# Kernel tuning notes

Measured on AMD Instinct MI355X. Metric: run time of the kernel, lower is better.

## Reference

```python
import jax, jax.numpy as jnp
import numpy as np

N = 500_000   # active voxel sites
C = 128       # inplanes == outplanes
K = 4         # 2x2 submanifold filter offsets
EPS = 1e-4    # SCN BatchNorm default eps


def setup_inputs() -> dict:
    key = jax.random.key(0)
    ks = jax.random.split(key, 10)
    feat = jax.random.normal(ks[0], (N, C), jnp.float32)
    in_idx = jax.random.randint(ks[1], (K, N), 0, N, dtype=jnp.int32)
    out_idx = jax.random.randint(ks[2], (K, N), 0, N, dtype=jnp.int32)
    mask = jax.random.randint(ks[3], (K, N), 0, 2, dtype=jnp.int32)
    scale = 1.0 / np.sqrt(K * C)
    W1 = jax.random.normal(ks[4], (K, C, C), jnp.float32) * scale
    W2 = jax.random.normal(ks[5], (K, C, C), jnp.float32) * scale
    gamma1 = jnp.ones((C,), jnp.float32)
    beta1 = jnp.zeros((C,), jnp.float32)
    mean1 = jax.random.normal(ks[6], (C,), jnp.float32) * 0.1
    var1 = jax.random.uniform(ks[7], (C,), jnp.float32, 0.5, 1.5)
    gamma2 = jnp.ones((C,), jnp.float32)
    beta2 = jnp.zeros((C,), jnp.float32)
    mean2 = jax.random.normal(ks[8], (C,), jnp.float32) * 0.1
    var2 = jax.random.uniform(ks[9], (C,), jnp.float32, 0.5, 1.5)
    return dict(feat=feat, W1=W1, W2=W2, gamma1=gamma1, beta1=beta1,
                mean1=mean1, var1=var1, gamma2=gamma2, beta2=beta2,
                mean2=mean2, var2=var2, in_idx=in_idx, out_idx=out_idx, mask=mask)


def _subm_conv(feat, W, in_idx, out_idx, maskf):
    # rulebook gather -> GEMM -> scatter-add, one pass per kernel offset
    out = jnp.zeros((feat.shape[0], W.shape[-1]), feat.dtype)
    for k in range(W.shape[0]):  # K=4 fixed small offsets
        g = feat[in_idx[k]] * maskf[k][:, None]   # [N, Cin]
        out = out.at[out_idx[k]].add(g @ W[k])    # scatter to active sites
    return out


def _bn(x, gamma, beta, mean, var):
    return (x - mean) * jax.lax.rsqrt(var + EPS) * gamma + beta


def reference(feat, W1, W2, gamma1, beta1, mean1, var1,
              gamma2, beta2, mean2, var2, in_idx, out_idx, mask):
    maskf = mask.astype(feat.dtype)
    residual = feat                              # scn.Identity (stride=1)
    h = _subm_conv(feat, W1, in_idx, out_idx, maskf)
    h = jax.nn.relu(_bn(h, gamma1, beta1, mean1, var1))  # BatchNormReLU
    h = _subm_conv(h, W2, in_idx, out_idx, maskf)
    h = _bn(h, gamma2, beta2, mean2, var2)       # BatchNormalization
    return h + residual                          # AddTable
```

## Files before the change

### kernel.cpp

```cpp
#include <hip/hip_runtime.h>

#define CDIM 128
#define KOFF 4
#define EPS 1e-4f
#define SCAN_CHUNK 2048
#define ROWS 32
#define NBLK 512
#define NTHR 512
#define CAPM (1 << 18)

typedef __attribute__((ext_vector_type(8))) short bf16x8;
typedef __attribute__((ext_vector_type(4))) float f32x4;

__device__ __forceinline__ unsigned short f2bf(float f) {
    unsigned int u = __builtin_bit_cast(unsigned int, f);
    u += 0x7fffu + ((u >> 16) & 1u);
    return (unsigned short)(u >> 16);
}
__device__ __forceinline__ float bf2f(unsigned short h) {
    unsigned int u = ((unsigned int)h) << 16;
    return __builtin_bit_cast(float, u);
}

__device__ __forceinline__ void gload_lds16(const void* g, void* l) {
    __builtin_amdgcn_global_load_lds(
        (const __attribute__((address_space(1))) void*)g,
        (__attribute__((address_space(3))) void*)l, 16, 0, 0);
}

__global__ __launch_bounds__(256) void wconv_kernel(
    const float* __restrict__ W1, const float* __restrict__ W2,
    short* __restrict__ W1t, short* __restrict__ W2t)
{
    int idx = blockIdx.x * 256 + threadIdx.x;
    if (idx >= KOFF * CDIM * CDIM) return;
    int ci = idx & (CDIM - 1);
    int co = (idx >> 7) & (CDIM - 1);
    int k  = idx >> 14;
    size_t src = (size_t)k * CDIM * CDIM + (size_t)ci * CDIM + co;
    W1t[idx] = (short)f2bf(W1[src]);
    W2t[idx] = (short)f2bf(W2[src]);
}

__global__ __launch_bounds__(256) void cvt_kernel(
    const float* __restrict__ in, short* __restrict__ out, size_t total8)
{
    size_t stride = (size_t)gridDim.x * 256;
    for (size_t i = (size_t)blockIdx.x * 256 + threadIdx.x; i < total8; i += stride) {
        float4 a = ((const float4*)in)[i * 2];
        float4 b = ((const float4*)in)[i * 2 + 1];
        bf16x8 v;
        v[0] = (short)f2bf(a.x); v[1] = (short)f2bf(a.y);
        v[2] = (short)f2bf(a.z); v[3] = (short)f2bf(a.w);
        v[4] = (short)f2bf(b.x); v[5] = (short)f2bf(b.y);
        v[6] = (short)f2bf(b.z); v[7] = (short)f2bf(b.w);
        ((bf16x8*)out)[i] = v;
    }
}

__global__ __launch_bounds__(256) void count_kernel(
    const int* __restrict__ out_idx, const int* __restrict__ mask,
    int* __restrict__ cnt, int n)
{
    int i = blockIdx.x * 256 + threadIdx.x;
    if (i >= n) return;
    int k = blockIdx.y;
    size_t s = (size_t)k * n + i;
    if (mask[s]) atomicAdd(&cnt[(size_t)out_idx[s] * KOFF + k], 1);
}

__global__ __launch_bounds__(256) void scan_p1(
    const int* __restrict__ in, int* __restrict__ bsum, int* __restrict__ bsum2, int L)
{
    __shared__ int red[256], red2[256];
    int base = blockIdx.x * SCAN_CHUNK;
    int s = 0, m = 0;
    #pragma unroll
    for (int u = 0; u < 8; ++u) {
        int i = base + u * 256 + threadIdx.x;
        if (i < L) { int v = in[i]; s += v; m += (v >= 2); }
    }
    red[threadIdx.x] = s; red2[threadIdx.x] = m;
    __syncthreads();
    for (int d = 128; d > 0; d >>= 1) {
        if (threadIdx.x < d) {
            red[threadIdx.x]  += red[threadIdx.x + d];
            red2[threadIdx.x] += red2[threadIdx.x + d];
        }
        __syncthreads();
    }
    if (threadIdx.x == 0) { bsum[blockIdx.x] = red[0]; bsum2[blockIdx.x] = red2[0]; }
}

__global__ __launch_bounds__(1024) void scan_p2(
    int* __restrict__ bsum, int* __restrict__ bsum2, int NB)
{
    __shared__ int s[1024], s2[1024];
    int t = threadIdx.x;
    s[t]  = (t < NB) ? bsum[t]  : 0;
    s2[t] = (t < NB) ? bsum2[t] : 0;
    __syncthreads();
    for (int d = 1; d < 1024; d <<= 1) {
        int x = s[t], y = s2[t];
        if (t >= d) { x += s[t - d]; y += s2[t - d]; }
        __syncthreads();
        s[t] = x; s2[t] = y;
        __syncthreads();
    }
    if (t < NB) {
        bsum[t]  = (t == 0) ? 0 : s[t - 1];
        bsum2[t] = (t == 0) ? 0 : s2[t - 1];
    }
}

__global__ __launch_bounds__(256) void scan_p3(
    const int* __restrict__ cnt, const int* __restrict__ bsum,
    const int* __restrict__ bsum2, int* __restrict__ off_start,
    int* __restrict__ fcur, int* __restrict__ prim,
    int* __restrict__ mlist, int* __restrict__ nmulti, int L, int KN)
{
    __shared__ int ts[256], ms[256];
    int t = threadIdx.x;
    int base = blockIdx.x * SCAN_CHUNK + t * 8;
    int v[8]; int s = 0, m = 0;
    #pragma unroll
    for (int u = 0; u < 8; ++u) {
        int i = base + u;
        v[u] = (i < L) ? cnt[i] : 0;
        s += v[u]; m += (v[u] >= 2);
    }
    ts[t] = s; ms[t] = m;
    __syncthreads();
    for (int d = 1; d < 256; d <<= 1) {
        int x = ts[t], y = ms[t];
        if (t >= d) { x += ts[t - d]; y += ms[t - d]; }
        __syncthreads();
        ts[t] = x; ms[t] = y;
        __syncthreads();
    }
    int pre  = bsum[blockIdx.x]  + ((t == 0) ? 0 : ts[t - 1]);
    int mpre = bsum2[blockIdx.x] + ((t == 0) ? 0 : ms[t - 1]);
    #pragma unroll
    for (int u = 0; u < 8; ++u) {
        int i = base + u;
        if (i < L) {
            off_start[i] = pre;
            fcur[i] = pre;
            if (i < KN) {
                int c = v[u];
                if (c == 0) prim[i] = -1;
                else if (c >= 2) {
                    if (mpre < CAPM) { prim[i] = 0x40000000 | mpre; mlist[mpre] = i; }
                    else prim[i] = -1;
                }
            } else {
                nmulti[0] = mpre;
            }
            pre += v[u]; mpre += (v[u] >= 2);
        }
    }
}

__global__ __launch_bounds__(256) void fill_kernel(
    const int* __restrict__ out_idx, const int* __restrict__ in_idx,
    const int* __restrict__ mask, const int* __restrict__ cnt,
    int* __restrict__ fcur, int* __restrict__ ent, int* __restrict__ prim, int n)
{
    int i = blockIdx.x * 256 + threadIdx.x;
    if (i >= n) return;
    int k = blockIdx.y;
    size_t s = (size_t)k * n + i;
    if (mask[s]) {
        int j = out_idx[s];
        size_t b = (size_t)j * KOFF + k;
        int src = in_idx[s];
        if (cnt[b] == 1) prim[b] = src;
        else { int pos = atomicAdd(&fcur[b], 1); ent[pos] = src; }
    }
}

__global__ __launch_bounds__(256) void merge_kernel(
    const short* __restrict__ Xb, const int* __restrict__ off_start,
    const int* __restrict__ ent, const int* __restrict__ mlist,
    const int* __restrict__ nmulti, short* __restrict__ sumbuf)
{
    int nm = *nmulti; if (nm > CAPM) nm = CAPM;
    int grp  = (blockIdx.x * 256 + threadIdx.x) >> 5;
    int gl   = threadIdx.x & 31;
    int ngrp = (gridDim.x * 256) >> 5;
    for (int i = grp; i < nm; i += ngrp) {
        int b  = mlist[i];
        int e0 = off_start[b];
        int e1 = off_start[b + 1];
        float a0 = 0.f, a1 = 0.f, a2 = 0.f, a3 = 0.f;
        for (int e = e0; e < e1; ++e) {
            int src = ent[e];
            ushort4 v = *((const ushort4*)(Xb + (size_t)src * CDIM) + gl);
            a0 += bf2f(v.x); a1 += bf2f(v.y); a2 += bf2f(v.z); a3 += bf2f(v.w);
        }
        ushort4 o;
        o.x = f2bf(a0); o.y = f2bf(a1); o.z = f2bf(a2); o.w = f2bf(a3);
        *((ushort4*)(sumbuf + (size_t)i * CDIM) + gl) = o;
    }
}

template <int EPI>
__global__ __launch_bounds__(NTHR, 4) void conv_kernel(
    const short* __restrict__ Xb, const short* __restrict__ sumbuf,
    const short* __restrict__ Wt, const int* __restrict__ prim,
    const char* __restrict__ zpage,
    const float* __restrict__ gamma, const float* __restrict__ beta,
    const float* __restrict__ mean, const float* __restrict__ var,
    const float* __restrict__ feat, void* __restrict__ Yv,
    int n, int ntile, int tpb)
{
    const int t    = threadIdx.x;
    const int w    = t >> 6;
    const int lane = t & 63;

    __shared__ alignas(16) short As[2][ROWS * 512];
    __shared__ alignas(16) float s_scale[CDIM], s_shift[CDIM];

    if (t < CDIM) {
        float sc = gamma[t] * rsqrtf(var[t] + EPS);
        s_scale[t] = sc;
        s_shift[t] = beta[t] - mean[t] * sc;
    }
    __syncthreads();

    int t0 = blockIdx.x * tpb;
    int t1 = min(t0 + tpb, ntile);
    if (t0 >= t1) return;

    const int q    = lane >> 4;
    const int p    = lane & 15;
    const int lrow = lane & 15;
    const int g2   = lane >> 4;

    bf16x8 wfr[16];
    #pragma unroll
    for (int ks = 0; ks < 16; ++ks) {
        int k  = ks >> 2;
        int kk = ks & 3;
        wfr[ks] = *(const bf16x8*)(Wt + (size_t)k * CDIM * CDIM
                                   + (w * 16 + lrow) * CDIM + kk * 32 + g2 * 8);
    }

    auto STAGE = [&](int ti, int buf) {
        int j0 = ti * ROWS;
        #pragma unroll
        for (int i = 0; i < 4; ++i) {
            int jl = w * 4 + i;
            int j  = j0 + jl;
            int pr = (j < n) ? prim[(size_t)j * KOFF + q] : -1;
            int boff = ((p ^ (jl & 7)) << 4);
            const char* g;
            if (pr < 0)               g = zpage + boff;
            else if (pr & 0x40000000) g = (const char*)sumbuf + ((size_t)(pr & 0x3FFFFFFF) << 8) + boff;
            else                      g = (const char*)Xb + ((size_t)pr << 8) + boff;
            gload_lds16(g, (char*)As[buf] + jl * 1024);
        }
    };

    STAGE(t0, 0);
    int cur = 0;
    for (int ti = t0; ti < t1; ++ti) {
        const int j0 = ti * ROWS;

        float4 fpre[2];
        if (EPI == 1) {
            #pragma unroll
            for (int u = 0; u < 2; ++u) {
                int idx = u * NTHR + t;
                int row = idx >> 5, c4 = idx & 31;
                int grow = j0 + row;
                fpre[u] = (grow < n) ? ((const float4*)feat)[(size_t)grow * 32 + c4]
                                     : make_float4(0.f, 0.f, 0.f, 0.f);
            }
        }

        if (ti + 1 < t1) {
            STAGE(ti + 1, cur ^ 1);
            if (ti == t0) {
                if (EPI == 1) asm volatile("s_waitcnt vmcnt(6)" ::: "memory");
                else          asm volatile("s_waitcnt vmcnt(4)" ::: "memory");
            } else {
                if (EPI == 1) asm volatile("s_waitcnt vmcnt(8)" ::: "memory");
                else          asm volatile("s_waitcnt vmcnt(6)" ::: "memory");
            }
        } else {
            asm volatile("s_waitcnt vmcnt(0)" ::: "memory");
        }
        __builtin_amdgcn_s_barrier();
        __builtin_amdgcn_sched_barrier(0);

        f32x4 acc[2];
        acc[0] = (f32x4){0.f, 0.f, 0.f, 0.f};
        acc[1] = (f32x4){0.f, 0.f, 0.f, 0.f};

        #pragma unroll
        for (int ks = 0; ks < 16; ++ks) {
            int cb = ks * 4 + g2;
            #pragma unroll
            for (int mt = 0; mt < 2; ++mt) {
                int row = mt * 16 + lrow;
                bf16x8 a = *(const bf16x8*)(&As[cur][row * 512 + ((cb ^ (row & 7)) << 3)]);
                acc[mt] = __builtin_amdgcn_mfma_f32_16x16x32_bf16(a, wfr[ks], acc[mt], 0, 0, 0);
            }
        }
        asm volatile("s_waitcnt lgkmcnt(0)" ::: "memory");
        __builtin_amdgcn_s_barrier();

        float* Ot = (float*)As[cur];
        #pragma unroll
        for (int mt = 0; mt < 2; ++mt)
            #pragma unroll
            for (int jj = 0; jj < 4; ++jj)
                Ot[(mt * 16 + g2 * 4 + jj) * 132 + w * 16 + lrow] = acc[mt][jj];
        asm volatile("s_waitcnt lgkmcnt(0)" ::: "memory");
        __builtin_amdgcn_s_barrier();

        #pragma unroll
        for (int u = 0; u < 2; ++u) {
            int idx = u * NTHR + t;
            int row = idx >> 5, c4 = idx & 31;
            int grow = j0 + row;
            if (grow < n) {
                float4 x  = *(const float4*)(Ot + row * 132 + c4 * 4);
                float4 sc = ((const float4*)s_scale)[c4];
                float4 sh = ((const float4*)s_shift)[c4];
                size_t go = (size_t)grow * 32 + c4;
                if (EPI == 0) {
                    ushort4 o;
                    o.x = f2bf(fmaxf(x.x * sc.x + sh.x, 0.f));
                    o.y = f2bf(fmaxf(x.y * sc.y + sh.y, 0.f));
                    o.z = f2bf(fmaxf(x.z * sc.z + sh.z, 0.f));
                    o.w = f2bf(fmaxf(x.w * sc.w + sh.w, 0.f));
                    ((ushort4*)Yv)[go] = o;
                } else {
                    float4 f = fpre[u];
                    float4 r;
                    r.x = x.x * sc.x + sh.x + f.x;
                    r.y = x.y * sc.y + sh.y + f.y;
                    r.z = x.z * sc.z + sh.z + f.z;
                    r.w = x.w * sc.w + sh.w + f.w;
                    ((float4*)Yv)[go] = r;
                }
            }
        }
        asm volatile("s_waitcnt lgkmcnt(0)" ::: "memory");
        __builtin_amdgcn_s_barrier();
        cur ^= 1;
    }
}

extern "C" void kernel_launch(void* const* d_in, const int* in_sizes, int n_in,
                              void* d_out, int out_size, void* d_ws, size_t ws_size,
                              hipStream_t stream)
{
    const float* feat   = (const float*)d_in[0];
    const float* W1     = (const float*)d_in[1];
    const float* W2     = (const float*)d_in[2];
    const float* gamma1 = (const float*)d_in[3];
    const float* beta1  = (const float*)d_in[4];
    const float* mean1  = (const float*)d_in[5];
    const float* var1   = (const float*)d_in[6];
    const float* gamma2 = (const float*)d_in[7];
    const float* beta2  = (const float*)d_in[8];
    const float* mean2  = (const float*)d_in[9];
    const float* var2   = (const float*)d_in[10];
    const int* in_idx   = (const int*)d_in[11];
    const int* out_idx  = (const int*)d_in[12];
    const int* mask     = (const int*)d_in[13];

    const int n  = in_sizes[0] / CDIM;
    const int KN = KOFF * n;
    const int L  = KN + 1;
    const int NB = (L + SCAN_CHUNK - 1) / SCAN_CHUNK;
    const size_t nelem = (size_t)n * CDIM;

    auto alignup = [](size_t x) { return (x + 255) & ~(size_t)255; };
    char* p = (char*)d_ws;
    int*   cnt    = (int*)p;    p += alignup((size_t)L * 4);
    int*   offs   = (int*)p;    p += alignup((size_t)L * 4);
    int*   fcur   = (int*)p;    p += alignup((size_t)L * 4);
    int*   bsum   = (int*)p;    p += alignup(4096 * 4);
    int*   bsum2  = (int*)p;    p += alignup(4096 * 4);
    int*   ent    = (int*)p;    p += alignup((size_t)KN * 4);
    int*   prim   = (int*)p;    p += alignup((size_t)KN * 4);
    int*   mlist  = (int*)p;    p += alignup((size_t)CAPM * 4);
    int*   nmulti = (int*)p;    p += 256;
    short* W1t    = (short*)p;  p += alignup((size_t)KOFF * CDIM * CDIM * 2);
    short* W2t    = (short*)p;  p += alignup((size_t)KOFF * CDIM * CDIM * 2);
    char*  zpage  = p;          p += 256;
    short* sumbuf = (short*)p;  p += alignup((size_t)CAPM * CDIM * 2);
    short* h1b    = (short*)p;
    short* fb     = (short*)d_out;

    hipMemsetAsync(cnt, 0, (size_t)L * 4, stream);
    hipMemsetAsync(zpage, 0, 256, stream);
    wconv_kernel<<<(KOFF * CDIM * CDIM + 255) / 256, 256, 0, stream>>>(W1, W2, W1t, W2t);
    cvt_kernel<<<2048, 256, 0, stream>>>(feat, fb, nelem / 8);
    dim3 cg((n + 255) / 256, KOFF);
    count_kernel<<<cg, 256, 0, stream>>>(out_idx, mask, cnt, n);
    scan_p1<<<NB, 256, 0, stream>>>(cnt, bsum, bsum2, L);
    scan_p2<<<1, 1024, 0, stream>>>(bsum, bsum2, NB);
    scan_p3<<<NB, 256, 0, stream>>>(cnt, bsum, bsum2, offs, fcur, prim, mlist, nmulti, L, KN);
    fill_kernel<<<cg, 256, 0, stream>>>(out_idx, in_idx, mask, cnt, fcur, ent, prim, n);

    const int ntile = (n + ROWS - 1) / ROWS;
    const int tpb   = (ntile + NBLK - 1) / NBLK;

    merge_kernel<<<1024, 256, 0, stream>>>(fb, offs, ent, mlist, nmulti, sumbuf);
    conv_kernel<0><<<NBLK, NTHR, 0, stream>>>(
        fb, sumbuf, W1t, prim, zpage, gamma1, beta1, mean1, var1, nullptr, h1b, n, ntile, tpb);
    merge_kernel<<<1024, 256, 0, stream>>>(h1b, offs, ent, mlist, nmulti, sumbuf);
    conv_kernel<1><<<NBLK, NTHR, 0, stream>>>(
        h1b, sumbuf, W2t, prim, zpage, gamma2, beta2, mean2, var2, feat, d_out, n, ntile, tpb);
}
```

Before: 741.8 us.

## Prefetch rulebook indices a tile ahead and write final epilogue directly from registers

The rulebook index loads for the next-next tile are now issued a tile early, so the gather addresses are ready when the async LDS staging is issued, and the vmcnt waits are adjusted to match. For the final (EPI==1) pass, the epilogue skips the LDS transpose and its two barriers: it applies BN, adds the residual and writes fp32 output straight from the MFMA accumulators, with the residual loaded per column. MFMA sections are also wrapped in s_setprio. The cost is scalar, less coalesced 4-byte stores and residual loads, and hand-tuned waitcnt values that must exactly match the number of outstanding loads.

```diff
diff --git a/kernel.cpp b/kernel.cpp
--- a/kernel.cpp
+++ b/kernel.cpp
@@ -236,6 +236,10 @@
     const int p    = lane & 15;
     const int lrow = lane & 15;
     const int g2   = lane >> 4;
+    const int col  = w * 16 + lrow;
+
+    const float csc = s_scale[col];
+    const float csh = s_shift[col];
 
     bf16x8 wfr[16];
     #pragma unroll
@@ -246,48 +250,56 @@
                                    + (w * 16 + lrow) * CDIM + kk * 32 + g2 * 8);
     }
 
-    auto STAGE = [&](int ti, int buf) {
+    auto LOADP = [&](int ti, int* pr) {
         int j0 = ti * ROWS;
         #pragma unroll
         for (int i = 0; i < 4; ++i) {
+            int j  = j0 + w * 4 + i;
+            int jc = (j < n) ? j : (n - 1);
+            int pv = prim[(size_t)jc * KOFF + q];
+            pr[i] = (j < n) ? pv : -1;
+        }
+    };
+    auto STAGE = [&](const int* pr, int buf) {
+        #pragma unroll
+        for (int i = 0; i < 4; ++i) {
             int jl = w * 4 + i;
-            int j  = j0 + jl;
-            int pr = (j < n) ? prim[(size_t)j * KOFF + q] : -1;
             int boff = ((p ^ (jl & 7)) << 4);
+            int pv = pr[i];
             const char* g;
-            if (pr < 0)               g = zpage + boff;
-            else if (pr & 0x40000000) g = (const char*)sumbuf + ((size_t)(pr & 0x3FFFFFFF) << 8) + boff;
-            else                      g = (const char*)Xb + ((size_t)pr << 8) + boff;
+            if (pv < 0)               g = zpage + boff;
+            else if (pv & 0x40000000) g = (const char*)sumbuf + ((size_t)(pv & 0x3FFFFFFF) << 8) + boff;
+            else                      g = (const char*)Xb + ((size_t)pv << 8) + boff;
             gload_lds16(g, (char*)As[buf] + jl * 1024);
         }
     };
 
-    STAGE(t0, 0);
+    int pcur[4], pnext[4];
+    LOADP(t0, pcur);
+    STAGE(pcur, 0);
+    LOADP(t0 + 1, pnext);
+
     int cur = 0;
     for (int ti = t0; ti < t1; ++ti) {
         const int j0 = ti * ROWS;
 
-        float4 fpre[2];
+        float fres[8];
         if (EPI == 1) {
             #pragma unroll
-            for (int u = 0; u < 2; ++u) {
-                int idx = u * NTHR + t;
-                int row = idx >> 5, c4 = idx & 31;
-                int grow = j0 + row;
-                fpre[u] = (grow < n) ? ((const float4*)feat)[(size_t)grow * 32 + c4]
-                                     : make_float4(0.f, 0.f, 0.f, 0.f);
-            }
+            for (int mt = 0; mt < 2; ++mt)
+                #pragma unroll
+                for (int jj = 0; jj < 4; ++jj) {
+                    int row = j0 + mt * 16 + g2 * 4 + jj;
+                    int rc  = (row < n) ? row : (n - 1);
+                    fres[mt * 4 + jj] = feat[(size_t)rc * CDIM + col];
+                }
         }
 
         if (ti + 1 < t1) {
-            STAGE(ti + 1, cur ^ 1);
-            if (ti == t0) {
-                if (EPI == 1) asm volatile("s_waitcnt vmcnt(6)" ::: "memory");
-                else          asm volatile("s_waitcnt vmcnt(4)" ::: "memory");
-            } else {
-                if (EPI == 1) asm volatile("s_waitcnt vmcnt(8)" ::: "memory");
-                else          asm volatile("s_waitcnt vmcnt(6)" ::: "memory");
-            }
+            STAGE(pnext, cur ^ 1);
+            LOADP(ti + 2, pnext);
+            if (EPI == 1) asm volatile("s_waitcnt vmcnt(16)" ::: "memory");
+            else          asm volatile("s_waitcnt vmcnt(8)"  ::: "memory");
         } else {
             asm volatile("s_waitcnt vmcnt(0)" ::: "memory");
         }
@@ -298,6 +310,7 @@
         acc[0] = (f32x4){0.f, 0.f, 0.f, 0.f};
         acc[1] = (f32x4){0.f, 0.f, 0.f, 0.f};
 
+        __builtin_amdgcn_s_setprio(1);
         #pragma unroll
         for (int ks = 0; ks < 16; ++ks) {
             int cb = ks * 4 + g2;
@@ -308,48 +321,53 @@
                 acc[mt] = __builtin_amdgcn_mfma_f32_16x16x32_bf16(a, wfr[ks], acc[mt], 0, 0, 0);
             }
         }
-        asm volatile("s_waitcnt lgkmcnt(0)" ::: "memory");
-        __builtin_amdgcn_s_barrier();
-
-        float* Ot = (float*)As[cur];
-        #pragma unroll
-        for (int mt = 0; mt < 2; ++mt)
+        __builtin_amdgcn_s_setprio(0);
+
+        if (EPI == 1) {
+            asm volatile("s_waitcnt lgkmcnt(0)" ::: "memory");
+            float* out = (float*)Yv;
             #pragma unroll
-            for (int jj = 0; jj < 4; ++jj)
-                Ot[(mt * 16 + g2 * 4 + jj) * 132 + w * 16 + lrow] = acc[mt][jj];
-        asm volatile("s_waitcnt lgkmcnt(0)" ::: "memory");
-        __builtin_amdgcn_s_barrier();
-
-        #pragma unroll
-        for (int u = 0; u < 2; ++u) {
-            int idx = u * NTHR + t;
-            int row = idx >> 5, c4 = idx & 31;
-            int grow = j0 + row;
-            if (grow < n) {
-                float4 x  = *(const float4*)(Ot + row * 132 + c4 * 4);
-                float4 sc = ((const float4*)s_scale)[c4];
-                float4 sh = ((const float4*)s_shift)[c4];
-                size_t go = (size_t)grow * 32 + c4;
-                if (EPI == 0) {
+            for (int mt = 0; mt < 2; ++mt)
+                #pragma unroll
+                for (int jj = 0; jj < 4; ++jj) {
+                    int row = j0 + mt * 16 + g2 * 4 + jj;
+                    if (row < n)
+                        out[(size_t)row * CDIM + col] =
+                            acc[mt][jj] * csc + csh + fres[mt * 4 + jj];
+                }
+            __builtin_amdgcn_s_barrier();
+        } else {
+            asm volatile("s_waitcnt lgkmcnt(0)" ::: "memory");
+            __builtin_amdgcn_s_barrier();
+            float* Ot = (float*)As[cur];
+            #pragma unroll
+            for (int mt = 0; mt < 2; ++mt)
+                #pragma unroll
+                for (int jj = 0; jj < 4; ++jj)
+                    Ot[(mt * 16 + g2 * 4 + jj) * 132 + col] = acc[mt][jj];
+            asm volatile("s_waitcnt lgkmcnt(0)" ::: "memory");
+            __builtin_amdgcn_s_barrier();
+
+            #pragma unroll
+            for (int u = 0; u < 2; ++u) {
+                int idx = u * NTHR + t;
+                int row = idx >> 5, c4 = idx & 31;
+                int grow = j0 + row;
+                if (grow < n) {
+                    float4 x  = *(const float4*)(Ot + row * 132 + c4 * 4);
+                    float4 sc = ((const float4*)s_scale)[c4];
+                    float4 sh = ((const float4*)s_shift)[c4];
                     ushort4 o;
                     o.x = f2bf(fmaxf(x.x * sc.x + sh.x, 0.f));
                     o.y = f2bf(fmaxf(x.y * sc.y + sh.y, 0.f));
                     o.z = f2bf(fmaxf(x.z * sc.z + sh.z, 0.f));
                     o.w = f2bf(fmaxf(x.w * sc.w + sh.w, 0.f));
-                    ((ushort4*)Yv)[go] = o;
-                } else {
-                    float4 f = fpre[u];
-                    float4 r;
-                    r.x = x.x * sc.x + sh.x + f.x;
-                    r.y = x.y * sc.y + sh.y + f.y;
-                    r.z = x.z * sc.z + sh.z + f.z;
-                    r.w = x.w * sc.w + sh.w + f.w;
-                    ((float4*)Yv)[go] = r;
+                    ((ushort4*)Yv)[(size_t)grow * 32 + c4] = o;
                 }
             }
-        }
-        asm volatile("s_waitcnt lgkmcnt(0)" ::: "memory");
-        __builtin_amdgcn_s_barrier();
+            asm volatile("s_waitcnt lgkmcnt(0)" ::: "memory");
+            __builtin_amdgcn_s_barrier();
+        }
         cur ^= 1;
     }
 }
```

Measured after the change: 708.2 us. 4.5% less time.

## Deepen conv gather pipeline to four stages with 16-row tiles and fuse prep kernels

Applied to the files above, without the earlier changes.

The conv kernel now uses 16-row tiles, four LDS buffers and a software pipeline that loads rulebook indices ahead of the async gather, so more global-to-LDS gathers are in flight per block. MFMA sections run at raised wave priority. The feature bf16 conversion and the count kernel are merged into one launch. The change drops the residual prefetch and assumes n divides by 16 (ntile = n/ROWS). It also hand-tunes vmcnt waits, which are fragile if the load counts change.

```diff
diff --git a/kernel.cpp b/kernel.cpp
--- a/kernel.cpp
+++ b/kernel.cpp
@@ -4,7 +4,8 @@
 #define KOFF 4
 #define EPS 1e-4f
 #define SCAN_CHUNK 2048
-#define ROWS 32
+#define ROWS 16
+#define NBUF 4
 #define NBLK 512
 #define NTHR 512
 #define CAPM (1 << 18)
@@ -42,31 +43,30 @@
     W2t[idx] = (short)f2bf(W2[src]);
 }
 
-__global__ __launch_bounds__(256) void cvt_kernel(
-    const float* __restrict__ in, short* __restrict__ out, size_t total8)
-{
-    size_t stride = (size_t)gridDim.x * 256;
-    for (size_t i = (size_t)blockIdx.x * 256 + threadIdx.x; i < total8; i += stride) {
-        float4 a = ((const float4*)in)[i * 2];
-        float4 b = ((const float4*)in)[i * 2 + 1];
-        bf16x8 v;
-        v[0] = (short)f2bf(a.x); v[1] = (short)f2bf(a.y);
-        v[2] = (short)f2bf(a.z); v[3] = (short)f2bf(a.w);
-        v[4] = (short)f2bf(b.x); v[5] = (short)f2bf(b.y);
-        v[6] = (short)f2bf(b.z); v[7] = (short)f2bf(b.w);
-        ((bf16x8*)out)[i] = v;
-    }
-}
-
-__global__ __launch_bounds__(256) void count_kernel(
+__global__ __launch_bounds__(256) void prep_kernel(
     const int* __restrict__ out_idx, const int* __restrict__ mask,
-    int* __restrict__ cnt, int n)
-{
-    int i = blockIdx.x * 256 + threadIdx.x;
-    if (i >= n) return;
-    int k = blockIdx.y;
-    size_t s = (size_t)k * n + i;
-    if (mask[s]) atomicAdd(&cnt[(size_t)out_idx[s] * KOFF + k], 1);
+    int* __restrict__ cnt, const float* __restrict__ feat,
+    short* __restrict__ fb, int n, size_t total8)
+{
+    if (blockIdx.y == KOFF) {
+        size_t stride = (size_t)gridDim.x * 256;
+        for (size_t i = (size_t)blockIdx.x * 256 + threadIdx.x; i < total8; i += stride) {
+            float4 a = ((const float4*)feat)[i * 2];
+            float4 b = ((const float4*)feat)[i * 2 + 1];
+            bf16x8 v;
+            v[0] = (short)f2bf(a.x); v[1] = (short)f2bf(a.y);
+            v[2] = (short)f2bf(a.z); v[3] = (short)f2bf(a.w);
+            v[4] = (short)f2bf(b.x); v[5] = (short)f2bf(b.y);
+            v[6] = (short)f2bf(b.z); v[7] = (short)f2bf(b.w);
+            ((bf16x8*)fb)[i] = v;
+        }
+    } else {
+        int i = blockIdx.x * 256 + threadIdx.x;
+        if (i >= n) return;
+        int k = blockIdx.y;
+        size_t s = (size_t)k * n + i;
+        if (mask[s]) atomicAdd(&cnt[(size_t)out_idx[s] * KOFF + k], 1);
+    }
 }
 
 __global__ __launch_bounds__(256) void scan_p1(
@@ -218,7 +218,7 @@
     const int w    = t >> 6;
     const int lane = t & 63;
 
-    __shared__ alignas(16) short As[2][ROWS * 512];
+    __shared__ alignas(16) short As[NBUF][ROWS * 512];
     __shared__ alignas(16) float s_scale[CDIM], s_shift[CDIM];
 
     if (t < CDIM) {
@@ -236,6 +236,7 @@
     const int p    = lane & 15;
     const int lrow = lane & 15;
     const int g2   = lane >> 4;
+    const int col  = w * 16 + lrow;
 
     bf16x8 wfr[16];
     #pragma unroll
@@ -246,85 +247,56 @@
                                    + (w * 16 + lrow) * CDIM + kk * 32 + g2 * 8);
     }
 
-    auto STAGE = [&](int ti, int buf) {
-        int j0 = ti * ROWS;
+    auto LOADP = [&](int ti, int* pr) {
+        int tc = (ti < t1) ? ti : (t1 - 1);
+        int j0 = tc * ROWS;
         #pragma unroll
-        for (int i = 0; i < 4; ++i) {
-            int jl = w * 4 + i;
-            int j  = j0 + jl;
-            int pr = (j < n) ? prim[(size_t)j * KOFF + q] : -1;
+        for (int i = 0; i < 2; ++i)
+            pr[i] = prim[(size_t)(j0 + w * 2 + i) * KOFF + q];
+    };
+    auto STAGE = [&](const int* pr, int buf) {
+        #pragma unroll
+        for (int i = 0; i < 2; ++i) {
+            int jl = w * 2 + i;
             int boff = ((p ^ (jl & 7)) << 4);
+            int pv = pr[i];
             const char* g;
-            if (pr < 0)               g = zpage + boff;
-            else if (pr & 0x40000000) g = (const char*)sumbuf + ((size_t)(pr & 0x3FFFFFFF) << 8) + boff;
-            else                      g = (const char*)Xb + ((size_t)pr << 8) + boff;
+            if (pv < 0)               g = zpage + boff;
+            else if (pv & 0x40000000) g = (const char*)sumbuf + ((size_t)(pv & 0x3FFFFFFF) << 8) + boff;
+            else                      g = (const char*)Xb + ((size_t)pv << 8) + boff;
             gload_lds16(g, (char*)As[buf] + jl * 1024);
         }
     };
 
-    STAGE(t0, 0);
-    int cur = 0;
-    for (int ti = t0; ti < t1; ++ti) {
-        const int j0 = ti * ROWS;
-
-        float4 fpre[2];
-        if (EPI == 1) {
-            #pragma unroll
-            for (int u = 0; u < 2; ++u) {
-                int idx = u * NTHR + t;
-                int row = idx >> 5, c4 = idx & 31;
-                int grow = j0 + row;
-                fpre[u] = (grow < n) ? ((const float4*)feat)[(size_t)grow * 32 + c4]
-                                     : make_float4(0.f, 0.f, 0.f, 0.f);
-            }
-        }
-
-        if (ti + 1 < t1) {
-            STAGE(ti + 1, cur ^ 1);
-            if (ti == t0) {
-                if (EPI == 1) asm volatile("s_waitcnt vmcnt(6)" ::: "memory");
-                else          asm volatile("s_waitcnt vmcnt(4)" ::: "memory");
-            } else {
-                if (EPI == 1) asm volatile("s_waitcnt vmcnt(8)" ::: "memory");
-                else          asm volatile("s_waitcnt vmcnt(6)" ::: "memory");
-            }
-        } else {
-            asm volatile("s_waitcnt vmcnt(0)" ::: "memory");
-        }
+    auto ITER = [&](int ti, int rb, int sb, const int* prS, int* prL, auto&& VMW) {
+        STAGE(prS, sb);
+        LOADP(ti + 4, prL);
+        VMW();
         __builtin_amdgcn_s_barrier();
         __builtin_amdgcn_sched_barrier(0);
 
-        f32x4 acc[2];
-        acc[0] = (f32x4){0.f, 0.f, 0.f, 0.f};
-        acc[1] = (f32x4){0.f, 0.f, 0.f, 0.f};
-
+        f32x4 acc = (f32x4){0.f, 0.f, 0.f, 0.f};
+        __builtin_amdgcn_s_setprio(1);
         #pragma unroll
         for (int ks = 0; ks < 16; ++ks) {
             int cb = ks * 4 + g2;
-            #pragma unroll
-            for (int mt = 0; mt < 2; ++mt) {
-                int row = mt * 16 + lrow;
-                bf16x8 a = *(const bf16x8*)(&As[cur][row * 512 + ((cb ^ (row & 7)) << 3)]);
-                acc[mt] = __builtin_amdgcn_mfma_f32_16x16x32_bf16(a, wfr[ks], acc[mt], 0, 0, 0);
-            }
-        }
+            bf16x8 a = *(const bf16x8*)(&As[rb][lrow * 512 + ((cb ^ (lrow & 7)) << 3)]);
+            acc = __builtin_amdgcn_mfma_f32_16x16x32_bf16(a, wfr[ks], acc, 0, 0, 0);
+        }
+        __builtin_amdgcn_s_setprio(0);
         asm volatile("s_waitcnt lgkmcnt(0)" ::: "memory");
         __builtin_amdgcn_s_barrier();
 
-        float* Ot = (float*)As[cur];
+        float* Ot = (float*)As[rb];
         #pragma unroll
-        for (int mt = 0; mt < 2; ++mt)
-            #pragma unroll
-            for (int jj = 0; jj < 4; ++jj)
-                Ot[(mt * 16 + g2 * 4 + jj) * 132 + w * 16 + lrow] = acc[mt][jj];
+        for (int jj = 0; jj < 4; ++jj)
+            Ot[(g2 * 4 + jj) * 132 + col] = acc[jj];
         asm volatile("s_waitcnt lgkmcnt(0)" ::: "memory");
         __builtin_amdgcn_s_barrier();
 
-        #pragma unroll
-        for (int u = 0; u < 2; ++u) {
-            int idx = u * NTHR + t;
-            int row = idx >> 5, c4 = idx & 31;
-            int grow = j0 + row;
+        {
+            int row = t >> 5, c4 = t & 31;
+            int grow = ti * ROWS + row;
             if (grow < n) {
                 float4 x  = *(const float4*)(Ot + row * 132 + c4 * 4);
                 float4 sc = ((const float4*)s_scale)[c4];
@@ -338,7 +310,7 @@
                     o.w = f2bf(fmaxf(x.w * sc.w + sh.w, 0.f));
                     ((ushort4*)Yv)[go] = o;
                 } else {
-                    float4 f = fpre[u];
+                    float4 f = ((const float4*)feat)[go];
                     float4 r;
                     r.x = x.x * sc.x + sh.x + f.x;
                     r.y = x.y * sc.y + sh.y + f.y;
@@ -350,8 +322,43 @@
         }
         asm volatile("s_waitcnt lgkmcnt(0)" ::: "memory");
         __builtin_amdgcn_s_barrier();
-        cur ^= 1;
-    }
+    };
+
+    #define VMW_LIT(N0, N1)                                                     \
+        [] {                                                                    \
+            if (EPI == 0) asm volatile("s_waitcnt vmcnt(" #N0 ")" ::: "memory");\
+            else          asm volatile("s_waitcnt vmcnt(" #N1 ")" ::: "memory");\
+        }
+
+    int p0[2], p1[2], p2[2], p3[2];
+    LOADP(t0,     p0);
+    LOADP(t0 + 1, p1);
+    LOADP(t0 + 2, p2);
+    STAGE(p0, 0);
+    STAGE(p1, 1);
+    STAGE(p2, 2);
+    LOADP(t0 + 3, p3);
+
+    ITER(t0 + 0, 0, 3, p3, p0, VMW_LIT(10, 10));
+    if (t0 + 1 < t1) {
+        ITER(t0 + 1, 1, 0, p0, p1, VMW_LIT(13, 14));
+        if (t0 + 2 < t1) {
+            ITER(t0 + 2, 2, 1, p1, p2, VMW_LIT(16, 18));
+            if (t0 + 3 < t1) {
+                ITER(t0 + 3, 3, 2, p2, p3, VMW_LIT(17, 20));
+                for (int ti = t0 + 4; ti < t1; ti += 4) {
+                    ITER(ti, 0, 3, p3, p0, VMW_LIT(17, 20));
+                    if (ti + 1 >= t1) break;
+                    ITER(ti + 1, 1, 0, p0, p1, VMW_LIT(17, 20));
+                    if (ti + 2 >= t1) break;
+                    ITER(ti + 2, 2, 1, p1, p2, VMW_LIT(17, 20));
+                    if (ti + 3 >= t1) break;
+                    ITER(ti + 3, 3, 2, p2, p3, VMW_LIT(17, 20));
+                }
+            }
+        }
+    }
+    #undef VMW_LIT
 }
 
 extern "C" void kernel_launch(void* const* d_in, const int* in_sizes, int n_in,
@@ -400,15 +407,15 @@
     hipMemsetAsync(cnt, 0, (size_t)L * 4, stream);
     hipMemsetAsync(zpage, 0, 256, stream);
     wconv_kernel<<<(KOFF * CDIM * CDIM + 255) / 256, 256, 0, stream>>>(W1, W2, W1t, W2t);
-    cvt_kernel<<<2048, 256, 0, stream>>>(feat, fb, nelem / 8);
-    dim3 cg((n + 255) / 256, KOFF);
-    count_kernel<<<cg, 256, 0, stream>>>(out_idx, mask, cnt, n);
+    dim3 pg((n + 255) / 256, KOFF + 1);
+    prep_kernel<<<pg, 256, 0, stream>>>(out_idx, mask, cnt, feat, fb, n, nelem / 8);
     scan_p1<<<NB, 256, 0, stream>>>(cnt, bsum, bsum2, L);
     scan_p2<<<1, 1024, 0, stream>>>(bsum, bsum2, NB);
     scan_p3<<<NB, 256, 0, stream>>>(cnt, bsum, bsum2, offs, fcur, prim, mlist, nmulti, L, KN);
-    fill_kernel<<<cg, 256, 0, stream>>>(out_idx, in_idx, mask, cnt, fcur, ent, prim, n);
-
-    const int ntile = (n + ROWS - 1) / ROWS;
+    dim3 fg((n + 255) / 256, KOFF);
+    fill_kernel<<<fg, 256, 0, stream>>>(out_idx, in_idx, mask, cnt, fcur, ent, prim, n);
+
+    const int ntile = n / ROWS;
     const int tpb   = (ntile + NBLK - 1) / NBLK;
 
     merge_kernel<<<1024, 256, 0, stream>>>(fb, offs, ent, mlist, nmulti, sumbuf);
```

Result: faster. 611.4 us (-17.6%).
